# Kernel optimization log

Hardware: AMD Instinct MI355X
Metric: run time of the kernel (lower is better)

## Reference

```python
import jax, jax.numpy as jnp
import numpy as np

B, S, D = 4, 2048, 1024

def _xavier(key, shape):
    bound = float(np.sqrt(6.0 / (shape[0] + shape[1])))
    return jax.random.uniform(key, shape, dtype=jnp.float32, minval=-bound, maxval=bound)

def setup_inputs() -> dict:
    key = jax.random.key(0)
    k0, k1, k2, k3 = jax.random.split(key, 4)
    return {
        "embeddings": jax.random.normal(k0, (B, S, D), dtype=jnp.float32),
        "W_Q": _xavier(k1, (D, D)),
        "W_K": _xavier(k2, (D, D)),
        "W_V": _xavier(k3, (D, D)),
    }

def reference(embeddings, W_Q, W_K, W_V):
    _, seq_len, d = embeddings.shape
    Q = embeddings @ W_Q                      # [B,S,D]
    K = embeddings @ W_K
    V = embeddings @ W_V
    scale = 1.0 / jnp.sqrt(jnp.float32(d))
    scores = jnp.einsum('bqd,bkd->bqk', Q, K) * scale   # [B,S,S]
    causal = jnp.tril(jnp.ones((seq_len, seq_len), dtype=bool))
    scores = jnp.where(causal[None, :, :], scores, -jnp.inf)
    probs = jax.nn.softmax(scores, axis=-1)
    return jnp.einsum('bqk,bkd->bqd', probs, V)
```

## Files before the change

### kernel.cpp

```cpp
#include <hip/hip_runtime.h>
#include <hip/hip_bf16.h>

#define BSZ 4
#define SEQ 2048
#define DIM 1024

typedef __attribute__((ext_vector_type(8))) short bf16x8;
typedef __attribute__((ext_vector_type(4))) float floatx4;

__device__ __forceinline__ unsigned short f2bf(float x) {
  union { float f; unsigned int u; } v; v.f = x;
  unsigned int r = v.u + 0x7fffu + ((v.u >> 16) & 1u);
  return (unsigned short)(r >> 16);
}

template <typename T> __device__ __forceinline__ void store_c(T* p, float v);
template <> __device__ __forceinline__ void store_c<float>(float* p, float v) { *p = v; }
template <> __device__ __forceinline__ void store_c<unsigned short>(unsigned short* p, float v) { *p = f2bf(v); }

__global__ __launch_bounds__(256) void cast_e(const float* __restrict__ in,
                                              unsigned short* __restrict__ out, int n) {
  int i = (blockIdx.x * 256 + threadIdx.x) * 4;
  if (i >= n) return;
  float4 v = *(const float4*)(in + i);
  ushort4 o;
  o.x = f2bf(v.x); o.y = f2bf(v.y); o.z = f2bf(v.z); o.w = f2bf(v.w);
  *(ushort4*)(out + i) = o;
}

__global__ __launch_bounds__(256) void transpose_w(const float* __restrict__ Wq,
                                                   const float* __restrict__ Wk,
                                                   const float* __restrict__ Wv,
                                                   unsigned short* __restrict__ WtQK,
                                                   unsigned short* __restrict__ WtV) {
  __shared__ float tile[32][33];
  int z = blockIdx.z;
  const float* W = (z == 0) ? Wq : (z == 1) ? Wk : Wv;
  unsigned short* dst = (z == 2) ? WtV : WtQK;
  int row_off = (z == 1) ? 1024 : 0;
  int n0 = blockIdx.x * 32, k0 = blockIdx.y * 32;
  int tx = threadIdx.x, ty = threadIdx.y;
  for (int r = ty; r < 32; r += 8)
    tile[r][tx] = W[(size_t)(k0 + r) * DIM + n0 + tx];
  __syncthreads();
  for (int r = ty; r < 32; r += 8)
    dst[(size_t)(row_off + n0 + r) * DIM + k0 + tx] = f2bf(tile[tx][r]);
}

__device__ __forceinline__ void gload16(const unsigned short* g, unsigned short* l) {
  __builtin_amdgcn_global_load_lds(
      (const __attribute__((address_space(1))) unsigned int*)g,
      (__attribute__((address_space(3))) unsigned int*)l, 16, 0, 0);
}

__device__ __forceinline__ void proj8ph(
    const unsigned short* __restrict__ A,
    const unsigned short* __restrict__ Bm,
    unsigned short* __restrict__ C, int ldc, int m0, int n0,
    unsigned short* sA, unsigned short* sB) {
  const int tid = threadIdx.x;
  const int lane = tid & 63;
  const int wid = tid >> 6;
  const int wm = (wid >> 2) * 128;
  const int wn = (wid & 3) * 64;
  const int lr = lane & 15, lq = lane >> 4;

  unsigned short* aB = sA + (wm >> 7) * 8192 + lr * 64;
  unsigned short* bB = sB + (wn >> 7) * 8192 + ((wn & 64) + lr) * 64;
  const int sw0 = (lq ^ (lr & 7)) * 8;
  const int sw1 = ((4 + lq) ^ (lr & 7)) * 8;

  const int schunk = (tid & 7) ^ ((tid >> 3) & 7);
  const unsigned short* gA = A + (size_t)(m0 + (tid >> 3)) * DIM + schunk * 8;
  const unsigned short* gB = Bm + (size_t)(n0 + (tid >> 3)) * DIM + schunk * 8;
  unsigned short* lA = sA + wid * 512;
  unsigned short* lB = sB + wid * 512;

#define STG_A(buf, T, half) do { \
    gload16(gA + (size_t)((half) * 128) * DIM + (T) * 64,      lA + (buf) * 16384 + (half) * 8192); \
    gload16(gA + (size_t)((half) * 128 + 64) * DIM + (T) * 64, lA + (buf) * 16384 + (half) * 8192 + 4096); } while (0)
#define STG_B(buf, T, half) do { \
    gload16(gB + (size_t)((half) * 128) * DIM + (T) * 64,      lB + (buf) * 16384 + (half) * 8192); \
    gload16(gB + (size_t)((half) * 128 + 64) * DIM + (T) * 64, lB + (buf) * 16384 + (half) * 8192 + 4096); } while (0)
#define RD_A(buf, qr) do { _Pragma("unroll") for (int i_ = 0; i_ < 4; ++i_) { \
    af[i_][0] = *(const bf16x8*)(aB + (buf) * 16384 + ((qr) * 64 + i_ * 16) * 64 + sw0); \
    af[i_][1] = *(const bf16x8*)(aB + (buf) * 16384 + ((qr) * 64 + i_ * 16) * 64 + sw1); } } while (0)
#define RD_B(buf, qc) do { _Pragma("unroll") for (int j_ = 0; j_ < 2; ++j_) { \
    bq[qc][j_][0] = *(const bf16x8*)(bB + (buf) * 16384 + ((qc) * 32 + j_ * 16) * 64 + sw0); \
    bq[qc][j_][1] = *(const bf16x8*)(bB + (buf) * 16384 + ((qc) * 32 + j_ * 16) * 64 + sw1); } } while (0)
#define MM(qr, qc) do { __builtin_amdgcn_s_setprio(1); \
    _Pragma("unroll") for (int i_ = 0; i_ < 4; ++i_) \
    _Pragma("unroll") for (int jj_ = 0; jj_ < 2; ++jj_) { \
      acc[(qr)*4+i_][(qc)*2+jj_] = __builtin_amdgcn_mfma_f32_16x16x32_bf16(af[i_][0], bq[qc][jj_][0], acc[(qr)*4+i_][(qc)*2+jj_], 0, 0, 0); \
      acc[(qr)*4+i_][(qc)*2+jj_] = __builtin_amdgcn_mfma_f32_16x16x32_bf16(af[i_][1], bq[qc][jj_][1], acc[(qr)*4+i_][(qc)*2+jj_], 0, 0, 0); } \
    __builtin_amdgcn_s_setprio(0); } while (0)
#define BAR __builtin_amdgcn_s_barrier()
#define LGKM0 do { asm volatile("s_waitcnt lgkmcnt(0)" ::: "memory"); __builtin_amdgcn_sched_barrier(0); } while (0)
#define VM4 asm volatile("s_waitcnt vmcnt(4)" ::: "memory")
#define VM0 asm volatile("s_waitcnt vmcnt(0)" ::: "memory")

  floatx4 acc[8][4] = {};
  bf16x8 af[4][2], bq[2][2][2];

  STG_B(0, 0, 0); STG_B(0, 0, 1);
  STG_A(0, 0, 0); STG_A(0, 0, 1);
  STG_B(1, 1, 0); STG_B(1, 1, 1);
  VM4;
  BAR;

#pragma unroll 1
  for (int j = 0; j < 8; ++j) {
    const int t0 = 2 * j, t1 = 2 * j + 1;
    const bool st = (j < 7);
    RD_A(0, 0); RD_B(0, 0);
    STG_A(1, t1, 0);
    BAR; LGKM0; MM(0, 0); BAR;

    RD_B(0, 1);
    STG_A(1, t1, 1);
    BAR; LGKM0; MM(0, 1); BAR;

    RD_A(0, 1);
    if (st) STG_B(0, t0 + 2, 0);
    BAR; LGKM0; MM(1, 0); BAR;

    if (st) STG_B(0, t0 + 2, 1);
    BAR; MM(1, 1);
    if (st) { VM4; } else { VM0; }
    BAR;

    RD_A(1, 0); RD_B(1, 0);
    if (st) STG_A(0, t0 + 2, 0);
    BAR; LGKM0; MM(0, 0); BAR;

    RD_B(1, 1);
    if (st) STG_A(0, t0 + 2, 1);
    BAR; LGKM0; MM(0, 1); BAR;

    RD_A(1, 1);
    if (st) STG_B(1, t1 + 2, 0);
    BAR; LGKM0; MM(1, 0); BAR;

    if (st) STG_B(1, t1 + 2, 1);
    BAR; MM(1, 1);
    if (st) { VM4; }
    BAR;
  }
#undef STG_A
#undef STG_B
#undef RD_A
#undef RD_B
#undef MM
#undef BAR
#undef LGKM0
#undef VM4
#undef VM0

#pragma unroll
  for (int i = 0; i < 8; ++i) {
    int rbase = m0 + wm + i * 16 + lq * 4;
#pragma unroll
    for (int jc = 0; jc < 4; ++jc) {
      int col = n0 + wn + jc * 16 + lr;
#pragma unroll
      for (int r = 0; r < 4; ++r)
        C[(size_t)(rbase + r) * ldc + col] = f2bf(acc[i][jc][r]);
    }
  }
}

#define NT_PROJ 32

template <int BMt>
__device__ __forceinline__ void proj_core(
    const unsigned short* __restrict__ A,
    const unsigned short* __restrict__ Bm,
    unsigned short* __restrict__ C, int ldc, int m0, int n0,
    unsigned short* sAr, unsigned short* sBr) {
  constexpr int LPA = BMt / 128;
  constexpr int LPT = LPA + 2;
  constexpr int FR  = BMt / 32;
  constexpr int TA  = BMt * 32;
  constexpr int TB  = 256 * 32;

  const int tid = threadIdx.x;
  const int lane = tid & 63;
  const int wid = tid >> 6;
  const int wm = (wid >> 2) * (BMt / 2);
  const int wn = (wid & 3) * 64;
  const int lr = lane & 15, lq = lane >> 4;

  const int srow = tid >> 2;
  const int schunk = (tid & 3) ^ ((tid >> 3) & 3);
  const unsigned short* gA = A + (size_t)(m0 + srow) * DIM + schunk * 8;
  const unsigned short* gB = Bm + (size_t)(n0 + srow) * DIM + schunk * 8;
  unsigned short* lA = sAr + 16 * 32 * wid;
  unsigned short* lB = sBr + 16 * 32 * wid;
  const size_t swG = (size_t)128 * DIM;

#define STAGE_A(T) do { int rb_ = (T) & 3; \
    gload16(gA + (size_t)(T) * 32, lA + rb_ * TA); \
    if constexpr (LPA == 2) gload16(gA + (size_t)(T) * 32 + swG, lA + rb_ * TA + 4096); } while (0)
#define STAGE_B(T) do { int rb_ = (T) & 3; \
    gload16(gB + (size_t)(T) * 32,       lB + rb_ * TB); \
    gload16(gB + (size_t)(T) * 32 + swG, lB + rb_ * TB + 4096); } while (0)
#define ARD(rb_, rowv) (*(const bf16x8*)&sAr[(rb_) * TA + (rowv) * 32 + (lq ^ (((rowv) >> 1) & 3)) * 8])
#define BRD(rb_, rowv) (*(const bf16x8*)&sBr[(rb_) * TB + (rowv) * 32 + (lq ^ (((rowv) >> 1) & 3)) * 8])

  floatx4 acc[FR][4] = {};

  STAGE_A(0); STAGE_B(0);
  STAGE_A(1); STAGE_B(1);
  STAGE_A(2); STAGE_B(2);
  if constexpr (LPT == 4) asm volatile("s_waitcnt vmcnt(8)" ::: "memory");
  else                    asm volatile("s_waitcnt vmcnt(6)" ::: "memory");
  __builtin_amdgcn_s_barrier();

#pragma unroll 4
  for (int T = 0; T < NT_PROJ; ++T) {
    const int rb = T & 3;
    bf16x8 af[4], bfr[4];
#pragma unroll
    for (int j = 0; j < 4; ++j) bfr[j] = BRD(rb, wn + j * 16 + lr);
#pragma unroll
    for (int i = 0; i < 4; ++i) af[i] = ARD(rb, wm + i * 16 + lr);
    if (T + 3 < NT_PROJ) {
      STAGE_A(T + 3);
      if constexpr (BMt == 128) STAGE_B(T + 3);
    }
    __builtin_amdgcn_s_barrier();
    __builtin_amdgcn_s_setprio(1);
#pragma unroll
    for (int i = 0; i < 4; ++i)
#pragma unroll
      for (int j = 0; j < 4; ++j)
        acc[i][j] = __builtin_amdgcn_mfma_f32_16x16x32_bf16(af[i], bfr[j], acc[i][j], 0, 0, 0);
    __builtin_amdgcn_s_setprio(0);
    if constexpr (BMt == 256) {
      __builtin_amdgcn_s_barrier();
#pragma unroll
      for (int i = 0; i < 4; ++i) af[i] = ARD(rb, wm + 64 + i * 16 + lr);
      if (T + 3 < NT_PROJ) STAGE_B(T + 3);
      __builtin_amdgcn_s_barrier();
      __builtin_amdgcn_s_setprio(1);
#pragma unroll
      for (int i = 0; i < 4; ++i)
#pragma unroll
        for (int j = 0; j < 4; ++j)
          acc[4 + i][j] = __builtin_amdgcn_mfma_f32_16x16x32_bf16(af[i], bfr[j], acc[4 + i][j], 0, 0, 0);
      __builtin_amdgcn_s_setprio(0);
    }
    if (T < NT_PROJ - 3) {
      if constexpr (LPT == 4) asm volatile("s_waitcnt vmcnt(8)" ::: "memory");
      else                    asm volatile("s_waitcnt vmcnt(6)" ::: "memory");
    } else if (T == NT_PROJ - 3) {
      if constexpr (LPT == 4) asm volatile("s_waitcnt vmcnt(4)" ::: "memory");
      else                    asm volatile("s_waitcnt vmcnt(3)" ::: "memory");
    } else if (T == NT_PROJ - 2) {
      asm volatile("s_waitcnt vmcnt(0)" ::: "memory");
    }
    __builtin_amdgcn_s_barrier();
  }
#undef STAGE_A
#undef STAGE_B
#undef ARD
#undef BRD

#pragma unroll
  for (int i = 0; i < FR; ++i) {
    int rbase = m0 + wm + i * 16 + lq * 4;
#pragma unroll
    for (int j = 0; j < 4; ++j) {
      int col = n0 + wn + j * 16 + lr;
#pragma unroll
      for (int r = 0; r < 4; ++r)
        C[(size_t)(rbase + r) * ldc + col] = f2bf(acc[i][j][r]);
    }
  }
}

__global__ __launch_bounds__(512, 2) void proj256(
    const unsigned short* __restrict__ Ebf,
    const unsigned short* __restrict__ WtQK,
    const unsigned short* __restrict__ WtV,
    unsigned short* __restrict__ QKo,
    unsigned short* __restrict__ Vt) {
  __shared__ __align__(16) unsigned short sA[32768];
  __shared__ __align__(16) unsigned short sB[32768];
  int x = blockIdx.x;
  if (x < 256) {
    proj8ph(Ebf, WtQK, QKo, 2 * DIM, (x >> 3) * 256, (x & 7) * 256, sA, sB);
  } else {
    x -= 256;
    proj_core<128>(WtV, Ebf, Vt, BSZ * SEQ, (x >> 5) * 128, (x & 31) * 256, sA, sB);
  }
}

template <typename OutT, int MODE>
__global__ __launch_bounds__(256) void gemm_nt(
    const unsigned short* __restrict__ A, int lda, long long strideA,
    const unsigned short* __restrict__ B, int ldb, long long strideB,
    OutT* __restrict__ C, int ldc, long long strideC,
    int Kdim, float scale, float* __restrict__ rowsum) {
  int m0, n0;
  if constexpr (MODE == 1) {
    int t = blockIdx.x;
    int mt = 0;
    while (((mt + 1) * (mt + 2)) / 2 <= t) mt++;
    int nt = t - (mt * (mt + 1)) / 2;
    m0 = mt * 128; n0 = nt * 128;
  } else {
    m0 = (gridDim.y - 1 - blockIdx.y) * 128;
    n0 = blockIdx.x * 128;
  }
  int Keff = (MODE == 2) ? min(Kdim, m0 + 128) : Kdim;
  A += (long long)blockIdx.z * strideA;
  B += (long long)blockIdx.z * strideB;
  C += (long long)blockIdx.z * strideC;
  rowsum += (size_t)blockIdx.z * SEQ;

  __shared__ __align__(16) unsigned short As[128][72];
  __shared__ __align__(16) unsigned short Bs[128][72];

  int tid = threadIdx.x;
  int lane = tid & 63;
  int wid = tid >> 6;
  int wm = (wid >> 1) * 64, wn = (wid & 1) * 64;
  int lr = lane & 15, lq = lane >> 4;
  int row = tid >> 3;
  int kc = (tid & 7) * 8;

  const unsigned short* Ab = A + (size_t)(m0 + row) * lda + kc;
  const unsigned short* Bb = B + (size_t)(n0 + row) * ldb + kc;
  size_t la = (size_t)32 * lda, lb = (size_t)32 * ldb;

  uint4 ra0 = *(const uint4*)(Ab);
  uint4 ra1 = *(const uint4*)(Ab + la);
  uint4 ra2 = *(const uint4*)(Ab + 2 * la);
  uint4 ra3 = *(const uint4*)(Ab + 3 * la);
  uint4 rb0 = *(const uint4*)(Bb);
  uint4 rb1 = *(const uint4*)(Bb + lb);
  uint4 rb2 = *(const uint4*)(Bb + 2 * lb);
  uint4 rb3 = *(const uint4*)(Bb + 3 * lb);

  floatx4 acc[4][4] = {};

  for (int k0 = 0; k0 < Keff; k0 += 64) {
    __syncthreads();
    *(uint4*)&As[row][kc]      = ra0;
    *(uint4*)&As[row + 32][kc] = ra1;
    *(uint4*)&As[row + 64][kc] = ra2;
    *(uint4*)&As[row + 96][kc] = ra3;
    *(uint4*)&Bs[row][kc]      = rb0;
    *(uint4*)&Bs[row + 32][kc] = rb1;
    *(uint4*)&Bs[row + 64][kc] = rb2;
    *(uint4*)&Bs[row + 96][kc] = rb3;
    if (k0 + 64 < Keff) {
      const unsigned short* An = Ab + k0 + 64;
      const unsigned short* Bn = Bb + k0 + 64;
      ra0 = *(const uint4*)(An);
      ra1 = *(const uint4*)(An + la);
      ra2 = *(const uint4*)(An + 2 * la);
      ra3 = *(const uint4*)(An + 3 * la);
      rb0 = *(const uint4*)(Bn);
      rb1 = *(const uint4*)(Bn + lb);
      rb2 = *(const uint4*)(Bn + 2 * lb);
      rb3 = *(const uint4*)(Bn + 3 * lb);
    }
    __syncthreads();
#pragma unroll
    for (int kk = 0; kk < 64; kk += 32) {
      bf16x8 af[4], bfr[4];
      int kl = kk + lq * 8;
#pragma unroll
      for (int i = 0; i < 4; i++) af[i] = *(const bf16x8*)&As[wm + i * 16 + lr][kl];
#pragma unroll
      for (int j = 0; j < 4; j++) bfr[j] = *(const bf16x8*)&Bs[wn + j * 16 + lr][kl];
#pragma unroll
      for (int i = 0; i < 4; i++)
#pragma unroll
        for (int j = 0; j < 4; j++)
          acc[i][j] = __builtin_amdgcn_mfma_f32_16x16x32_bf16(af[i], bfr[j], acc[i][j], 0, 0, 0);
    }
  }

  if constexpr (MODE == 1) {
#pragma unroll
    for (int i = 0; i < 4; i++) {
      int rbase = m0 + wm + i * 16 + lq * 4;
      float s0 = 0.f, s1 = 0.f, s2 = 0.f, s3 = 0.f;
#pragma unroll
      for (int j = 0; j < 4; j++) {
        int col = n0 + wn + j * 16 + lr;
        float e0 = (col <= rbase + 0) ? __expf(acc[i][j][0] * scale) : 0.0f;
        float e1 = (col <= rbase + 1) ? __expf(acc[i][j][1] * scale) : 0.0f;
        float e2 = (col <= rbase + 2) ? __expf(acc[i][j][2] * scale) : 0.0f;
        float e3 = (col <= rbase + 3) ? __expf(acc[i][j][3] * scale) : 0.0f;
        store_c(&C[(size_t)(rbase + 0) * ldc + col], e0);
        store_c(&C[(size_t)(rbase + 1) * ldc + col], e1);
        store_c(&C[(size_t)(rbase + 2) * ldc + col], e2);
        store_c(&C[(size_t)(rbase + 3) * ldc + col], e3);
        s0 += e0; s1 += e1; s2 += e2; s3 += e3;
      }
#pragma unroll
      for (int m = 1; m < 16; m <<= 1) {
        s0 += __shfl_xor(s0, m, 64);
        s1 += __shfl_xor(s1, m, 64);
        s2 += __shfl_xor(s2, m, 64);
        s3 += __shfl_xor(s3, m, 64);
      }
      if (lr == 0) {
        atomicAdd(&rowsum[rbase + 0], s0);
        atomicAdd(&rowsum[rbase + 1], s1);
        atomicAdd(&rowsum[rbase + 2], s2);
        atomicAdd(&rowsum[rbase + 3], s3);
      }
    }
  } else {
#pragma unroll
    for (int i = 0; i < 4; i++) {
      int rbase = m0 + wm + i * 16 + lq * 4;
      float i0 = 1.0f / rowsum[rbase + 0];
      float i1 = 1.0f / rowsum[rbase + 1];
      float i2 = 1.0f / rowsum[rbase + 2];
      float i3 = 1.0f / rowsum[rbase + 3];
#pragma unroll
      for (int j = 0; j < 4; j++) {
        int col = n0 + wn + j * 16 + lr;
        store_c(&C[(size_t)(rbase + 0) * ldc + col], acc[i][j][0] * i0);
        store_c(&C[(size_t)(rbase + 1) * ldc + col], acc[i][j][1] * i1);
        store_c(&C[(size_t)(rbase + 2) * ldc + col], acc[i][j][2] * i2);
        store_c(&C[(size_t)(rbase + 3) * ldc + col], acc[i][j][3] * i3);
      }
    }
  }
}

extern "C" void kernel_launch(void* const* d_in, const int* in_sizes, int n_in,
                              void* d_out, int out_size, void* d_ws, size_t ws_size,
                              hipStream_t stream) {
  const float* E  = (const float*)d_in[0];
  const float* Wq = (const float*)d_in[1];
  const float* Wk = (const float*)d_in[2];
  const float* Wv = (const float*)d_in[3];
  float* out = (float*)d_out;

  char* ws = (char*)d_ws;
  size_t off = 0;
  auto alloc = [&](size_t bytes) {
    void* p = ws + off;
    off += (bytes + 255) & ~(size_t)255;
    return p;
  };
  const size_t M_ALL = (size_t)BSZ * SEQ;
  unsigned short* Ebf  = (unsigned short*)alloc(M_ALL * DIM * 2);
  unsigned short* WtQK = (unsigned short*)alloc((size_t)2 * DIM * DIM * 2);
  unsigned short* WtV  = (unsigned short*)alloc((size_t)DIM * DIM * 2);
  unsigned short* QK   = (unsigned short*)alloc(M_ALL * 2 * DIM * 2);
  unsigned short* Vt   = (unsigned short*)alloc((size_t)DIM * M_ALL * 2);
  unsigned short* ExpS = (unsigned short*)alloc((size_t)BSZ * SEQ * SEQ * 2);
  float*          Rsum = (float*)alloc((size_t)BSZ * SEQ * 4);

  int nE = (int)(M_ALL * DIM);
  cast_e<<<dim3(nE / (256 * 4)), dim3(256), 0, stream>>>(E, Ebf, nE);
  transpose_w<<<dim3(32, 32, 3), dim3(32, 8), 0, stream>>>(Wq, Wk, Wv, WtQK, WtV);
  hipMemsetAsync(Rsum, 0, (size_t)BSZ * SEQ * 4, stream);

  proj256<<<dim3(512), dim3(512), 0, stream>>>(Ebf, WtQK, WtV, QK, Vt);

  gemm_nt<unsigned short, 1><<<dim3(136, 1, BSZ), dim3(256), 0, stream>>>(
      QK, 2 * DIM, (long long)SEQ * 2 * DIM,
      QK + DIM, 2 * DIM, (long long)SEQ * 2 * DIM,
      ExpS, SEQ, (long long)SEQ * SEQ,
      DIM, 0.03125f , Rsum);

  gemm_nt<float, 2><<<dim3(8, 16, BSZ), dim3(256), 0, stream>>>(
      ExpS, SEQ, (long long)SEQ * SEQ,
      Vt, (int)M_ALL, (long long)SEQ,
      out, DIM, (long long)SEQ * DIM,
      SEQ, 1.0f, Rsum);
}
```

Before: 243.7 us.

## Pipeline attention GEMMs with 4-stage async LDS ring and fold rowsum memset

Replaces the register-staged, double-barrier GEMM mainloop with a 4-deep ring of direct global-to-LDS loads (gload16), prefetching three k-tiles ahead. It uses XOR-swizzled LDS layout, explicit vmcnt waits and one barrier per stage, and raises MFMA priority with setprio. The rowsum zeroing moves from a separate hipMemsetAsync into the cast kernel to drop one launch. The k-step shrinks from 64 to 32 per stage, and correctness relies on the hand-tuned waitcnt counts matching the number of outstanding loads.

Measured after the change: 244.2 us. About the same (+0.2%).

```diff
diff --git a/kernel.cpp b/kernel.cpp
--- a/kernel.cpp
+++ b/kernel.cpp
@@ -19,7 +19,12 @@
 template <> __device__ __forceinline__ void store_c<unsigned short>(unsigned short* p, float v) { *p = f2bf(v); }
 
 __global__ __launch_bounds__(256) void cast_e(const float* __restrict__ in,
-                                              unsigned short* __restrict__ out, int n) {
+                                              unsigned short* __restrict__ out, int n,
+                                              float* __restrict__ rsum) {
+  if (blockIdx.x < 8) {
+    int j = blockIdx.x * 1024 + threadIdx.x * 4;
+    *(float4*)(rsum + j) = make_float4(0.f, 0.f, 0.f, 0.f);
+  }
   int i = (blockIdx.x * 256 + threadIdx.x) * 4;
   if (i >= n) return;
   float4 v = *(const float4*)(in + i);
@@ -297,7 +302,7 @@
 }
 
 template <typename OutT, int MODE>
-__global__ __launch_bounds__(256) void gemm_nt(
+__global__ __launch_bounds__(256, 2) void gemm_ring(
     const unsigned short* __restrict__ A, int lda, long long strideA,
     const unsigned short* __restrict__ B, int ldb, long long strideB,
     OutT* __restrict__ C, int ldc, long long strideC,
@@ -313,76 +318,67 @@
     m0 = (gridDim.y - 1 - blockIdx.y) * 128;
     n0 = blockIdx.x * 128;
   }
-  int Keff = (MODE == 2) ? min(Kdim, m0 + 128) : Kdim;
+  const int Keff = (MODE == 2) ? min(Kdim, m0 + 128) : Kdim;
+  const int NT = Keff >> 5;
   A += (long long)blockIdx.z * strideA;
   B += (long long)blockIdx.z * strideB;
   C += (long long)blockIdx.z * strideC;
   rowsum += (size_t)blockIdx.z * SEQ;
 
-  __shared__ __align__(16) unsigned short As[128][72];
-  __shared__ __align__(16) unsigned short Bs[128][72];
-
-  int tid = threadIdx.x;
-  int lane = tid & 63;
-  int wid = tid >> 6;
-  int wm = (wid >> 1) * 64, wn = (wid & 1) * 64;
-  int lr = lane & 15, lq = lane >> 4;
-  int row = tid >> 3;
-  int kc = (tid & 7) * 8;
-
-  const unsigned short* Ab = A + (size_t)(m0 + row) * lda + kc;
-  const unsigned short* Bb = B + (size_t)(n0 + row) * ldb + kc;
-  size_t la = (size_t)32 * lda, lb = (size_t)32 * ldb;
-
-  uint4 ra0 = *(const uint4*)(Ab);
-  uint4 ra1 = *(const uint4*)(Ab + la);
-  uint4 ra2 = *(const uint4*)(Ab + 2 * la);
-  uint4 ra3 = *(const uint4*)(Ab + 3 * la);
-  uint4 rb0 = *(const uint4*)(Bb);
-  uint4 rb1 = *(const uint4*)(Bb + lb);
-  uint4 rb2 = *(const uint4*)(Bb + 2 * lb);
-  uint4 rb3 = *(const uint4*)(Bb + 3 * lb);
+  __shared__ __align__(16) unsigned short sA[4 * 4096];
+  __shared__ __align__(16) unsigned short sB[4 * 4096];
+
+  const int tid = threadIdx.x;
+  const int lane = tid & 63;
+  const int wid = tid >> 6;
+  const int wm = (wid >> 1) * 64, wn = (wid & 1) * 64;
+  const int lr = lane & 15, lq = lane >> 4;
+
+  const int schunk = (tid & 3) ^ ((tid >> 3) & 3);
+  const unsigned short* gA = A + (size_t)(m0 + (tid >> 2)) * lda + schunk * 8;
+  const unsigned short* gB = B + (size_t)(n0 + (tid >> 2)) * ldb + schunk * 8;
+  unsigned short* lA = sA + wid * 512;
+  unsigned short* lB = sB + wid * 512;
+  const size_t sGA = (size_t)64 * lda, sGB = (size_t)64 * ldb;
+
+#define RSTAGE(T) do { int rb_ = (T) & 3; \
+    gload16(gA + (size_t)(T) * 32,       lA + rb_ * 4096); \
+    gload16(gA + (size_t)(T) * 32 + sGA, lA + rb_ * 4096 + 2048); \
+    gload16(gB + (size_t)(T) * 32,       lB + rb_ * 4096); \
+    gload16(gB + (size_t)(T) * 32 + sGB, lB + rb_ * 4096 + 2048); } while (0)
+#define RARD(rb_, rowv) (*(const bf16x8*)&sA[(rb_) * 4096 + (rowv) * 32 + (lq ^ (((rowv) >> 1) & 3)) * 8])
+#define RBRD(rb_, rowv) (*(const bf16x8*)&sB[(rb_) * 4096 + (rowv) * 32 + (lq ^ (((rowv) >> 1) & 3)) * 8])
 
   floatx4 acc[4][4] = {};
 
-  for (int k0 = 0; k0 < Keff; k0 += 64) {
-    __syncthreads();
-    *(uint4*)&As[row][kc]      = ra0;
-    *(uint4*)&As[row + 32][kc] = ra1;
-    *(uint4*)&As[row + 64][kc] = ra2;
-    *(uint4*)&As[row + 96][kc] = ra3;
-    *(uint4*)&Bs[row][kc]      = rb0;
-    *(uint4*)&Bs[row + 32][kc] = rb1;
-    *(uint4*)&Bs[row + 64][kc] = rb2;
-    *(uint4*)&Bs[row + 96][kc] = rb3;
-    if (k0 + 64 < Keff) {
-      const unsigned short* An = Ab + k0 + 64;
-      const unsigned short* Bn = Bb + k0 + 64;
-      ra0 = *(const uint4*)(An);
-      ra1 = *(const uint4*)(An + la);
-      ra2 = *(const uint4*)(An + 2 * la);
-      ra3 = *(const uint4*)(An + 3 * la);
-      rb0 = *(const uint4*)(Bn);
-      rb1 = *(const uint4*)(Bn + lb);
-      rb2 = *(const uint4*)(Bn + 2 * lb);
-      rb3 = *(const uint4*)(Bn + 3 * lb);
-    }
-    __syncthreads();
-#pragma unroll
-    for (int kk = 0; kk < 64; kk += 32) {
-      bf16x8 af[4], bfr[4];
-      int kl = kk + lq * 8;
-#pragma unroll
-      for (int i = 0; i < 4; i++) af[i] = *(const bf16x8*)&As[wm + i * 16 + lr][kl];
-#pragma unroll
-      for (int j = 0; j < 4; j++) bfr[j] = *(const bf16x8*)&Bs[wn + j * 16 + lr][kl];
-#pragma unroll
-      for (int i = 0; i < 4; i++)
-#pragma unroll
-        for (int j = 0; j < 4; j++)
-          acc[i][j] = __builtin_amdgcn_mfma_f32_16x16x32_bf16(af[i], bfr[j], acc[i][j], 0, 0, 0);
-    }
-  }
+  RSTAGE(0); RSTAGE(1); RSTAGE(2);
+  asm volatile("s_waitcnt vmcnt(8)" ::: "memory");
+  __builtin_amdgcn_s_barrier();
+
+  for (int T = 0; T < NT; ++T) {
+    const int rb = T & 3;
+    bf16x8 af[4], bfr[4];
+#pragma unroll
+    for (int j = 0; j < 4; ++j) bfr[j] = RBRD(rb, wn + j * 16 + lr);
+#pragma unroll
+    for (int i = 0; i < 4; ++i) af[i] = RARD(rb, wm + i * 16 + lr);
+    if (T + 3 < NT) RSTAGE(T + 3);
+    __builtin_amdgcn_s_barrier();
+    __builtin_amdgcn_s_setprio(1);
+#pragma unroll
+    for (int i = 0; i < 4; ++i)
+#pragma unroll
+      for (int j = 0; j < 4; ++j)
+        acc[i][j] = __builtin_amdgcn_mfma_f32_16x16x32_bf16(af[i], bfr[j], acc[i][j], 0, 0, 0);
+    __builtin_amdgcn_s_setprio(0);
+    if (T < NT - 3)       asm volatile("s_waitcnt vmcnt(8)" ::: "memory");
+    else if (T == NT - 3) asm volatile("s_waitcnt vmcnt(4)" ::: "memory");
+    else if (T == NT - 2) asm volatile("s_waitcnt vmcnt(0)" ::: "memory");
+    __builtin_amdgcn_s_barrier();
+  }
+#undef RSTAGE
+#undef RARD
+#undef RBRD
 
   if constexpr (MODE == 1) {
 #pragma unroll
@@ -462,19 +458,18 @@
   float*          Rsum = (float*)alloc((size_t)BSZ * SEQ * 4);
 
   int nE = (int)(M_ALL * DIM);
-  cast_e<<<dim3(nE / (256 * 4)), dim3(256), 0, stream>>>(E, Ebf, nE);
+  cast_e<<<dim3(nE / (256 * 4)), dim3(256), 0, stream>>>(E, Ebf, nE, Rsum);
   transpose_w<<<dim3(32, 32, 3), dim3(32, 8), 0, stream>>>(Wq, Wk, Wv, WtQK, WtV);
-  hipMemsetAsync(Rsum, 0, (size_t)BSZ * SEQ * 4, stream);
 
   proj256<<<dim3(512), dim3(512), 0, stream>>>(Ebf, WtQK, WtV, QK, Vt);
 
-  gemm_nt<unsigned short, 1><<<dim3(136, 1, BSZ), dim3(256), 0, stream>>>(
+  gemm_ring<unsigned short, 1><<<dim3(136, 1, BSZ), dim3(256), 0, stream>>>(
       QK, 2 * DIM, (long long)SEQ * 2 * DIM,
       QK + DIM, 2 * DIM, (long long)SEQ * 2 * DIM,
       ExpS, SEQ, (long long)SEQ * SEQ,
       DIM, 0.03125f , Rsum);
 
-  gemm_nt<float, 2><<<dim3(8, 16, BSZ), dim3(256), 0, stream>>>(
+  gemm_ring<float, 2><<<dim3(8, 16, BSZ), dim3(256), 0, stream>>>(
       ExpS, SEQ, (long long)SEQ * SEQ,
       Vt, (int)M_ALL, (long long)SEQ,
       out, DIM, (long long)SEQ * DIM,
```
